# Kernel optimization log

Hardware: AMD Instinct MI355X
Metric: run time of the kernel (lower is better)

Reference implementation:

```python
import jax, jax.numpy as jnp
import numpy as np

NUM_PATCHES = 16
FILTER_SIZE = 4
IN_CHANNELS = 64
OUT_CHANNELS = 256
BATCH = 64


def setup_inputs() -> dict:
    key = jax.random.key(0)
    k1, k2 = jax.random.split(key)
    D = NUM_PATCHES * FILTER_SIZE
    x = jax.random.normal(k1, (BATCH, IN_CHANNELS, D, D), dtype=jnp.float32)
    w = jax.random.normal(
        k2,
        (OUT_CHANNELS, IN_CHANNELS, NUM_PATCHES, NUM_PATCHES, FILTER_SIZE ** 2),
        dtype=jnp.float32,
    )
    return {"x": x, "w": w}


def reference(x, w):
    # x: (N, C, D, D) with D = P*f ; w: (O, C, P, P, f^2)
    N, C, D, _ = x.shape
    O, _, P, _, f2 = w.shape
    f = int(round(f2 ** 0.5))
    # non-overlapping unfold: (N,C,P,f,P,f) -> (N,C,P,P,f,f) -> (N,C,P,P,f^2)
    patches = x.reshape(N, C, P, f, P, f).transpose(0, 1, 2, 4, 3, 5).reshape(N, C, P, P, f2)
    # locally-connected contraction over in_channels and filter elements
    y = jnp.einsum('ncpqf,ocpqf->nopq', patches, w)
    scale = 1.0 / jnp.sqrt(jnp.asarray(f2 * C, dtype=x.dtype))
    return jax.nn.relu(y * scale)
```

## Files before the change

kernel.cpp:

```cpp
#include <hip/hip_runtime.h>


typedef short bf16x8 __attribute__((ext_vector_type(8)));
typedef float f32x4  __attribute__((ext_vector_type(4)));

__device__ __forceinline__ short f2bf(float f) {
    union { float f; unsigned u; } v; v.f = f;
    return (short)((v.u + 0x7FFFu + ((v.u >> 16) & 1u)) >> 16);
}

__device__ __forceinline__ bf16x8 pack8(f32x4 a, f32x4 b) {
    bf16x8 r;
    r[0] = f2bf(a[0]); r[1] = f2bf(a[1]); r[2] = f2bf(a[2]); r[3] = f2bf(a[3]);
    r[4] = f2bf(b[0]); r[5] = f2bf(b[1]); r[6] = f2bf(b[2]); r[7] = f2bf(b[3]);
    return r;
}

__device__ __forceinline__ void gload16(const void* g, void* l) {
    __builtin_amdgcn_global_load_lds(
        (const __attribute__((address_space(1))) void*)g,
        (__attribute__((address_space(3))) void*)l, 16, 0, 0);
}

__global__ __launch_bounds__(512)
void locblock_gemm(const float* __restrict__ x, const float* __restrict__ w,
                   float* __restrict__ ws) {
    __shared__ __align__(16) char smem[3][49152];

    const int hw = blockIdx.x;
    const int lb = (hw & 7) * 32 + (hw >> 3);
    const int p  = lb >> 4;
    const int q2 = (lb >> 1) & 7;
    const int oh = lb & 1;

    const int tid  = (int)threadIdx.x;
    const int lane = tid & 63;
    const int wv   = tid >> 6;
    const int l15  = lane & 15;
    const int kq   = lane >> 4;
    const int qw   = wv & 1;
    const int nc   = wv >> 1;

    const float* xsrc[2];
#pragma unroll
    for (int j = 0; j < 2; ++j) {
        const int id = j * 512 + tid;
        const int n = id >> 4, s = id & 15;
        const int u = s ^ (n & 15);
        xsrc[j] = x + (size_t)n * 262144u + (size_t)(u >> 3) * 4096u
                    + (size_t)(4 * p + ((u >> 1) & 3)) * 64u
                    + (size_t)(q2 * 8 + (u & 1) * 4);
    }
    const float* wsrc[4];
#pragma unroll
    for (int j = 0; j < 4; ++j) {
        const int id = j * 512 + tid;
        const int ol = id >> 4, s = id & 15;
        const int u = s ^ (ol & 15);
        wsrc[j] = w + (size_t)(oh * 128 + ol) * 262144u + (size_t)(u >> 3) * 4096u
                    + (size_t)p * 256u + (size_t)(q2 * 32) + (size_t)((u & 7) * 4);
    }

    int aoff[4][2], boff[2][2];
#pragma unroll
    for (int mf = 0; mf < 4; ++mf) {
        const int n = mf * 16 + l15;
        const int v1 = (kq >> 1) * 8 + (kq & 1) * 4 + qw;
        aoff[mf][0] = n * 256 + ((v1       ^ l15) * 16);
        aoff[mf][1] = n * 256 + (((v1 + 2) ^ l15) * 16);
    }
#pragma unroll
    for (int nf = 0; nf < 2; ++nf) {
        const int ol = nc * 32 + nf * 16 + l15;
        const int u1 = (kq >> 1) * 8 + qw * 4 + (kq & 1) * 2;
        boff[nf][0] = 16384 + ol * 256 + ((u1       ^ l15) * 16);
        boff[nf][1] = 16384 + ol * 256 + (((u1 + 1) ^ l15) * 16);
    }

    f32x4 acc[4][2];
#pragma unroll
    for (int mf = 0; mf < 4; ++mf)
#pragma unroll
        for (int nf = 0; nf < 2; ++nf)
            acc[mf][nf] = (f32x4){0.f, 0.f, 0.f, 0.f};

    auto stage = [&](int t, int buf) {
        char* base = smem[buf];
        const size_t toff = (size_t)t * 8192u;
#pragma unroll
        for (int j = 0; j < 2; ++j)
            gload16(xsrc[j] + toff, base + j * 8192 + wv * 1024);
#pragma unroll
        for (int j = 0; j < 4; ++j)
            gload16(wsrc[j] + toff, base + 16384 + j * 8192 + wv * 1024);
    };

    auto compute = [&](int buf) {
        const char* Lb = smem[buf];
        bf16x8 av[4], bv[2];
#pragma unroll
        for (int mf = 0; mf < 4; ++mf)
            av[mf] = pack8(*(const f32x4*)(Lb + aoff[mf][0]),
                           *(const f32x4*)(Lb + aoff[mf][1]));
#pragma unroll
        for (int nf = 0; nf < 2; ++nf)
            bv[nf] = pack8(*(const f32x4*)(Lb + boff[nf][0]),
                           *(const f32x4*)(Lb + boff[nf][1]));
#pragma unroll
        for (int mf = 0; mf < 4; ++mf)
#pragma unroll
            for (int nf = 0; nf < 2; ++nf)
                acc[mf][nf] = __builtin_amdgcn_mfma_f32_16x16x32_bf16(
                    av[mf], bv[nf], acc[mf][nf], 0, 0, 0);
    };

    stage(0, 0);
    stage(1, 1);
    stage(2, 2);
#pragma unroll 1
    for (int t = 0; t < 29; ++t) {
        const int buf = t % 3;
        asm volatile("s_waitcnt vmcnt(12)" ::: "memory");
        __builtin_amdgcn_s_barrier();
        compute(buf);
        asm volatile("s_waitcnt lgkmcnt(0)" ::: "memory");
        __builtin_amdgcn_s_barrier();
        stage(t + 3, buf);
    }
    asm volatile("s_waitcnt vmcnt(12)" ::: "memory");
    __builtin_amdgcn_s_barrier();
    compute(2);
    asm volatile("s_waitcnt vmcnt(6)" ::: "memory");
    __builtin_amdgcn_s_barrier();
    compute(0);
    asm volatile("s_waitcnt vmcnt(0)" ::: "memory");
    __builtin_amdgcn_s_barrier();
    compute(1);

    const float scale = 0.03125f;
    const int pq = p * 16 + q2 * 2 + qw;
#pragma unroll
    for (int mf = 0; mf < 4; ++mf)
#pragma unroll
        for (int nf = 0; nf < 2; ++nf) {
            const int o  = oh * 128 + nc * 32 + nf * 16 + l15;
            const int n0 = mf * 16 + kq * 4;
            f32x4 r;
#pragma unroll
            for (int j = 0; j < 4; ++j)
                r[j] = fmaxf(acc[mf][nf][j] * scale, 0.0f);
            *(f32x4*)(ws + (size_t)pq * 16384u + (size_t)o * 64u + n0) = r;
        }
}

__global__ __launch_bounds__(256)
void finish_transpose(const float* __restrict__ ws, float* __restrict__ out) {
    __shared__ float tile[256 * 68];
    const int o = blockIdx.x;
    const int t = (int)threadIdx.x;

#pragma unroll
    for (int it = 0; it < 16; ++it) {
        const int chunk = it * 256 + t;
        const int pq = chunk >> 4, ng = chunk & 15;
        const f32x4 v = *(const f32x4*)(ws + (size_t)pq * 16384u
                                           + (size_t)o * 64u + ng * 4);
        *(f32x4*)&tile[pq * 68 + ng * 4] = v;
    }
    __syncthreads();

    const int n = t >> 2, pqq = t & 3;
#pragma unroll
    for (int i = 0; i < 16; ++i) {
        const int pq0 = i * 16 + pqq * 4;
        f32x4 r;
#pragma unroll
        for (int k = 0; k < 4; ++k)
            r[k] = tile[(pq0 + k) * 68 + n];
        *(f32x4*)(out + (size_t)n * 65536u + (size_t)o * 256u + pq0) = r;
    }
}

extern "C" void kernel_launch(void* const* d_in, const int* in_sizes, int n_in,
                              void* d_out, int out_size, void* d_ws, size_t ws_size,
                              hipStream_t stream) {
    const float* x = (const float*)d_in[0];
    const float* w = (const float*)d_in[1];
    float* out = (float*)d_out;
    float* ws  = (float*)d_ws;
    locblock_gemm<<<dim3(256), dim3(512), 0, stream>>>(x, w, ws);
    finish_transpose<<<dim3(256), dim3(256), 0, stream>>>(ws, out);
}
```

Before: 90.84 us.

## Pre-unfold activations to bf16 in a patch-major layout before the GEMM

Adds a prep kernel that unfolds x into patch-major, bf16-packed tiles so the main GEMM loads activations as contiguous 16-byte bf16 fragments. This removes the per-iteration fp32-to-bf16 conversion and halves the LDS footprint and global traffic for the A operand inside the GEMM. In exchange it adds a third kernel launch plus an extra global write and read of the converted activations (about 32 MB of workspace), and the waitcnt values change to match the smaller load count.

```diff
diff --git a/kernel.cpp b/kernel.cpp
--- a/kernel.cpp
+++ b/kernel.cpp
@@ -2,6 +2,7 @@
 
 
 typedef short bf16x8 __attribute__((ext_vector_type(8)));
+typedef short bf16x4 __attribute__((ext_vector_type(4)));
 typedef float f32x4  __attribute__((ext_vector_type(4)));
 
 __device__ __forceinline__ short f2bf(float f) {
@@ -22,10 +23,43 @@
         (__attribute__((address_space(3))) void*)l, 16, 0, 0);
 }
 
+__global__ __launch_bounds__(256)
+void prep_unfold(const float* __restrict__ x, short* __restrict__ xT) {
+    __shared__ __align__(16) char tile[16 * 2056];
+    const int bid = blockIdx.x;
+    const int p = bid >> 6, c = bid & 63;
+    const int t = (int)threadIdx.x;
+
+#pragma unroll
+    for (int it = 0; it < 16; ++it) {
+        const int id = it * 256 + t;
+        const int n = id >> 6, fr = (id >> 4) & 3, cq = id & 15;
+        const f32x4 v = *(const f32x4*)(x + (size_t)n * 262144u
+                                          + (size_t)c * 4096u
+                                          + (size_t)(4 * p + fr) * 64u
+                                          + (size_t)(cq * 4));
+        bf16x4 b; b[0] = f2bf(v[0]); b[1] = f2bf(v[1]);
+                  b[2] = f2bf(v[2]); b[3] = f2bf(v[3]);
+        *(bf16x4*)(tile + cq * 2056 + (fr >> 1) * 1024 + n * 16
+                        + (fr & 1) * 8) = b;
+    }
+    __syncthreads();
+
+#pragma unroll
+    for (int it = 0; it < 8; ++it) {
+        const int id = it * 256 + t;
+        const int q = id >> 7, s = id & 127;
+        const int koct = s >> 6, n = s & 63;
+        const bf16x8 v = *(const bf16x8*)(tile + q * 2056 + koct * 1024 + n * 16);
+        *(bf16x8*)(xT + (size_t)(p * 16 + q) * 65536u + (size_t)c * 1024u
+                      + (size_t)koct * 512u + (size_t)n * 8u) = v;
+    }
+}
+
 __global__ __launch_bounds__(512)
-void locblock_gemm(const float* __restrict__ x, const float* __restrict__ w,
-                   float* __restrict__ ws) {
-    __shared__ __align__(16) char smem[3][49152];
+void locblock_gemm(const short* __restrict__ xT, const float* __restrict__ w,
+                   float* __restrict__ ws2) {
+    __shared__ __align__(16) char smem[3][41472];
 
     const int hw = blockIdx.x;
     const int lb = (hw & 7) * 32 + (hw >> 3);
@@ -41,16 +75,11 @@
     const int qw   = wv & 1;
     const int nc   = wv >> 1;
 
-    const float* xsrc[2];
-#pragma unroll
-    for (int j = 0; j < 2; ++j) {
-        const int id = j * 512 + tid;
-        const int n = id >> 4, s = id & 15;
-        const int u = s ^ (n & 15);
-        xsrc[j] = x + (size_t)n * 262144u + (size_t)(u >> 3) * 4096u
-                    + (size_t)(4 * p + ((u >> 1) & 3)) * 64u
-                    + (size_t)(q2 * 8 + (u & 1) * 4);
-    }
+    const int qin  = wv >> 2, acf = (wv >> 1) & 1, akoct = wv & 1;
+    const short* asrc = xT + (size_t)(p * 16 + q2 * 2 + qin) * 65536u
+                           + (size_t)acf * 1024u + (size_t)akoct * 512u
+                           + (size_t)lane * 8u;
+
     const float* wsrc[4];
 #pragma unroll
     for (int j = 0; j < 4; ++j) {
@@ -61,20 +90,18 @@
                     + (size_t)p * 256u + (size_t)(q2 * 32) + (size_t)((u & 7) * 4);
     }
 
-    int aoff[4][2], boff[2][2];
-#pragma unroll
-    for (int mf = 0; mf < 4; ++mf) {
-        const int n = mf * 16 + l15;
-        const int v1 = (kq >> 1) * 8 + (kq & 1) * 4 + qw;
-        aoff[mf][0] = n * 256 + ((v1       ^ l15) * 16);
-        aoff[mf][1] = n * 256 + (((v1 + 2) ^ l15) * 16);
-    }
-#pragma unroll
-    for (int nf = 0; nf < 2; ++nf) {
-        const int ol = nc * 32 + nf * 16 + l15;
+    int aoff[4], boff[2][2];
+#pragma unroll
+    for (int mf = 0; mf < 4; ++mf)
+        aoff[mf] = (qw * 4 + kq) * 1088 + (mf * 16 + l15) * 16;
+    {
         const int u1 = (kq >> 1) * 8 + qw * 4 + (kq & 1) * 2;
-        boff[nf][0] = 16384 + ol * 256 + ((u1       ^ l15) * 16);
-        boff[nf][1] = 16384 + ol * 256 + (((u1 + 1) ^ l15) * 16);
+#pragma unroll
+        for (int nf = 0; nf < 2; ++nf) {
+            const int ol = nc * 32 + nf * 16 + l15;
+            boff[nf][0] = 8704 + ol * 256 + ((u1       ^ l15) * 16);
+            boff[nf][1] = 8704 + ol * 256 + (((u1 + 1) ^ l15) * 16);
+        }
     }
 
     f32x4 acc[4][2];
@@ -86,13 +113,11 @@
 
     auto stage = [&](int t, int buf) {
         char* base = smem[buf];
-        const size_t toff = (size_t)t * 8192u;
-#pragma unroll
-        for (int j = 0; j < 2; ++j)
-            gload16(xsrc[j] + toff, base + j * 8192 + wv * 1024);
+        gload16(asrc + (size_t)t * 2048u, base + wv * 1088);
 #pragma unroll
         for (int j = 0; j < 4; ++j)
-            gload16(wsrc[j] + toff, base + 16384 + j * 8192 + wv * 1024);
+            gload16(wsrc[j] + (size_t)t * 8192u,
+                    base + 8704 + j * 8192 + wv * 1024);
     };
 
     auto compute = [&](int buf) {
@@ -100,8 +125,7 @@
         bf16x8 av[4], bv[2];
 #pragma unroll
         for (int mf = 0; mf < 4; ++mf)
-            av[mf] = pack8(*(const f32x4*)(Lb + aoff[mf][0]),
-                           *(const f32x4*)(Lb + aoff[mf][1]));
+            av[mf] = *(const bf16x8*)(Lb + aoff[mf]);
 #pragma unroll
         for (int nf = 0; nf < 2; ++nf)
             bv[nf] = pack8(*(const f32x4*)(Lb + boff[nf][0]),
@@ -120,17 +144,17 @@
 #pragma unroll 1
     for (int t = 0; t < 29; ++t) {
         const int buf = t % 3;
-        asm volatile("s_waitcnt vmcnt(12)" ::: "memory");
+        asm volatile("s_waitcnt vmcnt(10)" ::: "memory");
         __builtin_amdgcn_s_barrier();
         compute(buf);
         asm volatile("s_waitcnt lgkmcnt(0)" ::: "memory");
         __builtin_amdgcn_s_barrier();
         stage(t + 3, buf);
     }
-    asm volatile("s_waitcnt vmcnt(12)" ::: "memory");
+    asm volatile("s_waitcnt vmcnt(10)" ::: "memory");
     __builtin_amdgcn_s_barrier();
     compute(2);
-    asm volatile("s_waitcnt vmcnt(6)" ::: "memory");
+    asm volatile("s_waitcnt vmcnt(5)" ::: "memory");
     __builtin_amdgcn_s_barrier();
     compute(0);
     asm volatile("s_waitcnt vmcnt(0)" ::: "memory");
@@ -149,12 +173,12 @@
 #pragma unroll
             for (int j = 0; j < 4; ++j)
                 r[j] = fmaxf(acc[mf][nf][j] * scale, 0.0f);
-            *(f32x4*)(ws + (size_t)pq * 16384u + (size_t)o * 64u + n0) = r;
+            *(f32x4*)(ws2 + (size_t)pq * 16384u + (size_t)o * 64u + n0) = r;
         }
 }
 
 __global__ __launch_bounds__(256)
-void finish_transpose(const float* __restrict__ ws, float* __restrict__ out) {
+void finish_transpose(const float* __restrict__ ws2, float* __restrict__ out) {
     __shared__ float tile[256 * 68];
     const int o = blockIdx.x;
     const int t = (int)threadIdx.x;
@@ -163,8 +187,8 @@
     for (int it = 0; it < 16; ++it) {
         const int chunk = it * 256 + t;
         const int pq = chunk >> 4, ng = chunk & 15;
-        const f32x4 v = *(const f32x4*)(ws + (size_t)pq * 16384u
-                                           + (size_t)o * 64u + ng * 4);
+        const f32x4 v = *(const f32x4*)(ws2 + (size_t)pq * 16384u
+                                            + (size_t)o * 64u + ng * 4);
         *(f32x4*)&tile[pq * 68 + ng * 4] = v;
     }
     __syncthreads();
@@ -187,7 +211,9 @@
     const float* x = (const float*)d_in[0];
     const float* w = (const float*)d_in[1];
     float* out = (float*)d_out;
-    float* ws  = (float*)d_ws;
-    locblock_gemm<<<dim3(256), dim3(512), 0, stream>>>(x, w, ws);
-    finish_transpose<<<dim3(256), dim3(256), 0, stream>>>(ws, out);
-}
+    short* xT  = (short*)d_ws;
+    float* ws2 = (float*)((char*)d_ws + (33554432));
+    prep_unfold     <<<dim3(1024), dim3(256), 0, stream>>>(x, xT);
+    locblock_gemm   <<<dim3(256),  dim3(512), 0, stream>>>(xT, w, ws2);
+    finish_transpose<<<dim3(256),  dim3(256), 0, stream>>>(ws2, out);
+}
```

After: 104.8 us. 1.15x slower.
